# Kernel optimization log

Hardware: AMD Instinct MI355X
Metric: run time of the kernel (lower is better)

## Reference

```python
import jax, jax.numpy as jnp
import numpy as np

D_MODEL = 1024
HEADS = 16
SCALE = float(np.sqrt(D_MODEL / HEADS))  # sqrt(d_k) = sqrt(64) = 8


def setup_inputs() -> dict:
    key = jax.random.key(0)
    ks = jax.random.split(key, 5)
    B, S, D = 4, 2048, D_MODEL
    q = jax.random.normal(ks[0], (B, S, D), dtype=jnp.float32)
    init = 0.02
    wq = jax.random.normal(ks[1], (D, D), dtype=jnp.float32) * init
    wk = jax.random.normal(ks[2], (D, D), dtype=jnp.float32) * init
    wv = jax.random.normal(ks[3], (D, D), dtype=jnp.float32) * init
    wo = jax.random.normal(ks[4], (D, D), dtype=jnp.float32) * init
    return {"q": q, "wq": wq, "wk": wk, "wv": wv, "wo": wo}


def reference(q, wq, wk, wv, wo):
    # Faithful to the source: NO head split is ever performed.
    B, S, D = q.shape
    # nn.Linear convention: y = x @ W.T, weight is [out, in]
    Q = jnp.einsum('bsd,ed->bse', q, wq)
    K = jnp.einsum('bsd,ed->bse', q, wk)
    V = jnp.einsum('bsd,ed->bse', q, wv)
    scores = jnp.einsum('bqe,bke->bqk', Q, K) / SCALE  # [B, S, S]
    attn = jax.nn.softmax(scores, axis=-1)
    out = jnp.einsum('bqk,bke->bqe', attn, V)  # [B, S, D]
    # Source bug reproduced: transpose(1,2).contiguous().view(B, S, -1)
    # => reshape the [B, D, S] contiguous buffer back to [B, S, D].
    out = jnp.transpose(out, (0, 2, 1)).reshape(B, S, D)
    return jnp.einsum('bsd,ed->bse', out, wo)
```

## Files before the change

kernel.cpp:

```cpp
#include <hip/hip_runtime.h>
#include <hip/hip_bf16.h>
#include <stdint.h>

typedef __bf16 bf16;
typedef __attribute__((ext_vector_type(8))) __bf16 bf16x8;
typedef __attribute__((ext_vector_type(4))) float f32x4;
typedef __attribute__((ext_vector_type(8))) unsigned short u16x8;

#define LDS_U32 __attribute__((address_space(3))) uint32_t
#define GLB_U32 const __attribute__((address_space(1))) uint32_t
#define GLOAD16(g, l) __builtin_amdgcn_global_load_lds((GLB_U32*)(g), (LDS_U32*)(l), 16, 0, 0)

#define DSR(dst, addr, OFFLIT) \
  asm volatile("ds_read_b128 %0, %1 offset:" OFFLIT : "=v"(dst) : "v"(addr))

#define WAIT_LGKM0() asm volatile("s_waitcnt lgkmcnt(0)")
#define WAIT_VM(n)   asm volatile("s_waitcnt vmcnt(" #n ")")

__global__ __launch_bounds__(256) void cvt_all(const float* __restrict__ q,
                                               const float* __restrict__ wq,
                                               const float* __restrict__ wk,
                                               const float* __restrict__ wv,
                                               const float* __restrict__ wo,
                                               bf16* __restrict__ qb,
                                               bf16* __restrict__ W3,
                                               bf16* __restrict__ wob) {
  const int b = blockIdx.x;
  const float* src;
  bf16* dst;
  int within;
  if (b < 2048) { src = q; dst = qb; within = b; }
  else {
    const int seg = (b - 2048) >> 8;
    within = (b - 2048) & 255;
    if (seg == 0)      { src = wq; dst = W3; }
    else if (seg == 1) { src = wk; dst = W3 + 1048576; }
    else if (seg == 2) { src = wv; dst = W3 + 2097152; }
    else               { src = wo; dst = wob; }
  }
  const int off = within * 1024;
#pragma unroll
  for (int it = 0; it < 4; ++it) {
    const int j = off + it * 256 + threadIdx.x;
    float4 v = reinterpret_cast<const float4*>(src)[j];
    ushort4 o;
    o.x = __builtin_bit_cast(unsigned short, (bf16)v.x);
    o.y = __builtin_bit_cast(unsigned short, (bf16)v.y);
    o.z = __builtin_bit_cast(unsigned short, (bf16)v.z);
    o.w = __builtin_bit_cast(unsigned short, (bf16)v.w);
    reinterpret_cast<ushort4*>(dst)[j] = o;
  }
}

template <int EPI, int WN>
__global__ __launch_bounds__(512, 2) void g256(const bf16* __restrict__ A,
                                               const bf16* __restrict__ Bm,
                                               void* __restrict__ Cp,
                                               int K, float alpha,
                                               long sA, long sB, long sC, int ldc) {
  constexpr int BN = WN * 64;
  __shared__ bf16 smem_[(32768 + WN * 8192) / 2];
  const long z = blockIdx.z;
  const int t = threadIdx.x;
  const int l = t & 63;
  const int w = t >> 6;
  const int wr = (w >> 2) * 128;
  const int wc = (w & 3) * (WN * 16);
  const int NT = K >> 6;

  const bf16* Ab = A + z * sA + (long)(blockIdx.y * 256) * K;
  const bf16* Bb = Bm + z * sB + (long)(blockIdx.x * BN) * K;

  uint32_t loc = (uint32_t)t * 16u;
  uint32_t g0 = loc ^ (((loc >> 9) & 1u) << 5);
  const int r0 = (int)(((g0 >> 10) >> 1) * 16 + ((g0 >> 6) & 15));
  const int c0 = (int)(((g0 >> 10) & 1) * 32 + ((g0 & 63) >> 1));

  uint32_t lo_ = (uint32_t)((l & 15) * 64 + (l >> 4) * 16);
  const uint32_t lane_off = lo_ ^ (((lo_ >> 9) & 1u) << 5);
  const uint32_t aRegion = (uint32_t)(wr >> 7) * 16384u;
  const uint32_t smem_base = (uint32_t)(size_t)&smem_[0];
  const uint32_t aAddr = smem_base + aRegion + lane_off;

  uint32_t bA[WN];
#pragma unroll
  for (int n = 0; n < WN; ++n) {
    const uint32_t row = (uint32_t)(wc + n * 16);
    bA[n] = smem_base + 32768u + (row >> 6) * 8192u + ((row & 63u) >> 4) * 2048u + lane_off;
  }

  auto STAGE1 = [&](const bf16* mat, int unit, int tile, uint32_t isB) {
    uint32_t dst = isB + (uint32_t)unit * 8192u + (uint32_t)t * 16u;
    const bf16* src = mat + (long)(unit * 64 + r0) * K + tile * 64 + c0;
    GLOAD16(src, smem_ + (dst >> 1));
  };

  f32x4 acc[8][WN] = {};

  STAGE1(Ab, 0, 0, 0u); STAGE1(Ab, 1, 0, 0u); STAGE1(Ab, 2, 0, 0u); STAGE1(Ab, 3, 0, 0u);
#pragma unroll
  for (int u = 0; u < WN; ++u) STAGE1(Bb, u, 0, 32768u);
  __builtin_amdgcn_sched_barrier(0);
  WAIT_VM(0);
  __builtin_amdgcn_s_barrier();

#define MFMAPH(ph)                                                                   \
  _Pragma("unroll") for (int mi = 0; mi < 2; ++mi)                                   \
  _Pragma("unroll") for (int n = 0; n < WN; ++n)                                     \
  _Pragma("unroll") for (int kk = 0; kk < 2; ++kk)                                   \
    acc[(ph) * 2 + mi][n] = __builtin_amdgcn_mfma_f32_16x16x32_bf16(                 \
        __builtin_bit_cast(bf16x8, aF[mi][kk]), __builtin_bit_cast(bf16x8, bF[n][kk]), \
        acc[(ph) * 2 + mi][n], 0, 0, 0);

  for (int T = 0; T < NT; ++T) {
    f32x4 bF[WN][2];
    f32x4 aF[2][2];

#pragma unroll
    for (int n = 0; n < WN; ++n) {
      DSR(bF[n][0], bA[n], "0");
      DSR(bF[n][1], bA[n], "1024");
    }
    DSR(aF[0][0], aAddr, "0");    DSR(aF[0][1], aAddr, "1024");
    DSR(aF[1][0], aAddr, "2048"); DSR(aF[1][1], aAddr, "3072");
    __builtin_amdgcn_sched_barrier(0);
    __builtin_amdgcn_s_barrier();
    WAIT_LGKM0();
    __builtin_amdgcn_sched_barrier(0);
    __builtin_amdgcn_s_setprio(1);
    MFMAPH(0)
    __builtin_amdgcn_s_setprio(0);
    __builtin_amdgcn_s_barrier();

    {
      const uint32_t aP = aAddr + 4096u;
      DSR(aF[0][0], aP, "0");    DSR(aF[0][1], aP, "1024");
      DSR(aF[1][0], aP, "2048"); DSR(aF[1][1], aP, "3072");
      if (T + 1 < NT) {
#pragma unroll
        for (int u = 0; u < WN; ++u) STAGE1(Bb, u, T + 1, 32768u);
      }
      __builtin_amdgcn_sched_barrier(0);
      __builtin_amdgcn_s_barrier();
      WAIT_LGKM0();
      __builtin_amdgcn_sched_barrier(0);
      __builtin_amdgcn_s_setprio(1);
      MFMAPH(1)
      __builtin_amdgcn_s_setprio(0);
      __builtin_amdgcn_sched_barrier(0);
      if (T + 1 < NT) {
        if constexpr (WN == 2) { WAIT_VM(2); }
        else if constexpr (WN == 3) { WAIT_VM(3); }
        else { WAIT_VM(4); }
      } else {
        WAIT_VM(0);
      }
      __builtin_amdgcn_sched_barrier(0);
      __builtin_amdgcn_s_barrier();
    }

    {
      const uint32_t aP = aAddr + 8192u;
      DSR(aF[0][0], aP, "0");    DSR(aF[0][1], aP, "1024");
      DSR(aF[1][0], aP, "2048"); DSR(aF[1][1], aP, "3072");
      if (T + 1 < NT) { STAGE1(Ab, 0, T + 1, 0u); STAGE1(Ab, 2, T + 1, 0u); }
      __builtin_amdgcn_sched_barrier(0);
      __builtin_amdgcn_s_barrier();
      WAIT_LGKM0();
      __builtin_amdgcn_sched_barrier(0);
      __builtin_amdgcn_s_setprio(1);
      MFMAPH(2)
      __builtin_amdgcn_s_setprio(0);
      __builtin_amdgcn_s_barrier();
    }

    {
      const uint32_t aP = aAddr + 12288u;
      DSR(aF[0][0], aP, "0");    DSR(aF[0][1], aP, "1024");
      DSR(aF[1][0], aP, "2048"); DSR(aF[1][1], aP, "3072");
      __builtin_amdgcn_sched_barrier(0);
      __builtin_amdgcn_s_barrier();
      WAIT_LGKM0();
      __builtin_amdgcn_sched_barrier(0);
      __builtin_amdgcn_s_setprio(1);
      MFMAPH(3)
      __builtin_amdgcn_s_setprio(0);
      __builtin_amdgcn_s_barrier();
    }

    if (T + 1 < NT) { STAGE1(Ab, 1, T + 1, 0u); STAGE1(Ab, 3, T + 1, 0u); }
    __builtin_amdgcn_sched_barrier(0);
    if (T + 1 < NT) { WAIT_VM(2); } else { WAIT_VM(0); }
    __builtin_amdgcn_sched_barrier(0);
    __builtin_amdgcn_s_barrier();
  }
#undef MFMAPH

  const int orow0 = blockIdx.y * 256 + wr + (l >> 4) * 4;
  const int ocol0 = blockIdx.x * BN + wc + (l & 15);
#pragma unroll
  for (int m = 0; m < 8; ++m)
#pragma unroll
    for (int n = 0; n < WN; ++n)
#pragma unroll
      for (int i = 0; i < 4; ++i) {
        const long r = orow0 + m * 16 + i;
        const long c = ocol0 + n * 16;
        const float v = acc[m][n][i] * alpha;
        if constexpr (EPI == 0) {
          ((bf16*)Cp)[z * sC + r * ldc + c] = (bf16)v;
        } else if constexpr (EPI == 2) {
          ((float*)Cp)[r * ldc + c] = v;
        } else if constexpr (EPI == 4) {
          ((bf16*)Cp)[(r >> 11) * 2097152 + c * 2048 + (r & 2047)] = (bf16)v;
        } else {
          bf16* Qb = (bf16*)Cp;
          bf16* Kb = Qb + 8388608;
          if (c < 1024) Qb[r * 1024 + c] = (bf16)v;
          else Kb[r * 1024 + (c - 1024)] = (bf16)v;
        }
      }
}

__global__ __launch_bounds__(256) void softmax_rows(bf16* __restrict__ P) {
  const long row = blockIdx.x;
  bf16* p = P + row * 2048;
  const int t = threadIdx.x;
  const int lane = t & 63;
  const int wave = t >> 6;

  u16x8 raw = *reinterpret_cast<const u16x8*>(p + t * 8);
  float v[8];
#pragma unroll
  for (int j = 0; j < 8; ++j) {
    uint32_t bits = ((uint32_t)raw[j]) << 16;
    v[j] = __builtin_bit_cast(float, bits);
  }
  float m = v[0];
#pragma unroll
  for (int j = 1; j < 8; ++j) m = fmaxf(m, v[j]);
#pragma unroll
  for (int off = 32; off > 0; off >>= 1) m = fmaxf(m, __shfl_xor(m, off, 64));
  __shared__ float redm[4];
  __shared__ float reds[4];
  if (lane == 0) redm[wave] = m;
  __syncthreads();
  m = fmaxf(fmaxf(redm[0], redm[1]), fmaxf(redm[2], redm[3]));

  float s = 0.f;
#pragma unroll
  for (int j = 0; j < 8; ++j) {
    v[j] = __expf(v[j] - m);
    s += v[j];
  }
#pragma unroll
  for (int off = 32; off > 0; off >>= 1) s += __shfl_xor(s, off, 64);
  if (lane == 0) reds[wave] = s;
  __syncthreads();
  s = reds[0] + reds[1] + reds[2] + reds[3];
  const float inv = 1.f / s;

  u16x8 o;
#pragma unroll
  for (int j = 0; j < 8; ++j) o[j] = __builtin_bit_cast(unsigned short, (bf16)(v[j] * inv));
  *reinterpret_cast<u16x8*>(p + t * 8) = o;
}

extern "C" void kernel_launch(void* const* d_in, const int* in_sizes, int n_in,
                              void* d_out, int out_size, void* d_ws, size_t ws_size,
                              hipStream_t stream) {
  const float* q = (const float*)d_in[0];
  const float* wq = (const float*)d_in[1];
  const float* wk = (const float*)d_in[2];
  const float* wv = (const float*)d_in[3];
  const float* wo = (const float*)d_in[4];
  float* out = (float*)d_out;

  constexpr int B = 4, S = 2048, D = 1024;
  constexpr long SD = (long)S * D;
  constexpr long SS = (long)S * S;
  constexpr long DD = (long)D * D;

  bf16* wsb = (bf16*)d_ws;
  bf16* qb = wsb;
  bf16* W3 = qb + B * SD;
  bf16* wob = W3 + 3 * DD;
  bf16* Qb = wob + DD;
  bf16* Kb = Qb + B * SD;
  bf16* Vt = Kb + B * SD;
  bf16* P = Vt + B * SD;
  bf16* X = P + B * SS;

  cvt_all<<<3072, 256, 0, stream>>>(q, wq, wk, wv, wo, qb, W3, wob);

  g256<5, 4><<<dim3(8, 32, 1), 512, 0, stream>>>(qb, W3, Qb, D, 1.f, 0, 0, 0, 0);
  g256<4, 2><<<dim3(8, 32, 1), 512, 0, stream>>>(qb, W3 + 2 * DD, Vt, D, 1.f, 0, 0, 0, 0);
  g256<0, 4><<<dim3(8, 8, B), 512, 0, stream>>>(Qb, Kb, P, D, 0.125f, SD, SD, SS, S);
  softmax_rows<<<B * S, 256, 0, stream>>>(P);
  g256<0, 2><<<dim3(16, 4, B), 512, 0, stream>>>(Vt, P, X, S, 1.f, SD, SS, SD, S);
  g256<2, 2><<<dim3(8, 32, 1), 512, 0, stream>>>(X, wob, out, D, 1.f, 0, 0, 0, D);
}
```

Before: 207.4 us.

## Double-buffer GEMM LDS tiles and collapse per-phase barriers into one per K-step

The main GEMM kernel's single shared-memory tile is replaced by two ping-pong buffers indexed by K-tile parity. Global-to-LDS loads for tile T+1 are issued at the start of step T. The four MFMA phases become two larger phases of eight A fragment reads each. Only one vmcnt(0) wait and one barrier remain per K iteration, which removes most of the intra-iteration s_barrier synchronisation. The cost is double the LDS footprint, which may prevent two 512-thread blocks from fitting per CU as the launch bounds assume, and the finer-grained waves interleaving of the old schedule is lost.

```diff
diff --git a/kernel.cpp b/kernel.cpp
--- a/kernel.cpp
+++ b/kernel.cpp
@@ -15,7 +15,7 @@
   asm volatile("ds_read_b128 %0, %1 offset:" OFFLIT : "=v"(dst) : "v"(addr))
 
 #define WAIT_LGKM0() asm volatile("s_waitcnt lgkmcnt(0)")
-#define WAIT_VM(n)   asm volatile("s_waitcnt vmcnt(" #n ")")
+#define WAIT_VM0()   asm volatile("s_waitcnt vmcnt(0)")
 
 __global__ __launch_bounds__(256) void cvt_all(const float* __restrict__ q,
                                                const float* __restrict__ wq,
@@ -59,7 +59,8 @@
                                                int K, float alpha,
                                                long sA, long sB, long sC, int ldc) {
   constexpr int BN = WN * 64;
-  __shared__ bf16 smem_[(32768 + WN * 8192) / 2];
+  constexpr uint32_t PARB = 32768u + WN * 8192u;
+  __shared__ bf16 smem_[PARB];
   const long z = blockIdx.z;
   const int t = threadIdx.x;
   const int l = t & 63;
@@ -80,7 +81,7 @@
   const uint32_t lane_off = lo_ ^ (((lo_ >> 9) & 1u) << 5);
   const uint32_t aRegion = (uint32_t)(wr >> 7) * 16384u;
   const uint32_t smem_base = (uint32_t)(size_t)&smem_[0];
-  const uint32_t aAddr = smem_base + aRegion + lane_off;
+  const uint32_t aBase = smem_base + aRegion + lane_off;
 
   uint32_t bA[WN];
 #pragma unroll
@@ -90,7 +91,7 @@
   }
 
   auto STAGE1 = [&](const bf16* mat, int unit, int tile, uint32_t isB) {
-    uint32_t dst = isB + (uint32_t)unit * 8192u + (uint32_t)t * 16u;
+    uint32_t dst = (uint32_t)(tile & 1) * PARB + isB + (uint32_t)unit * 8192u + (uint32_t)t * 16u;
     const bf16* src = mat + (long)(unit * 64 + r0) * K + tile * 64 + c0;
     GLOAD16(src, smem_ + (dst >> 1));
   };
@@ -101,100 +102,73 @@
 #pragma unroll
   for (int u = 0; u < WN; ++u) STAGE1(Bb, u, 0, 32768u);
   __builtin_amdgcn_sched_barrier(0);
-  WAIT_VM(0);
+  WAIT_VM0();
   __builtin_amdgcn_s_barrier();
 
-#define MFMAPH(ph)                                                                   \
-  _Pragma("unroll") for (int mi = 0; mi < 2; ++mi)                                   \
-  _Pragma("unroll") for (int n = 0; n < WN; ++n)                                     \
-  _Pragma("unroll") for (int kk = 0; kk < 2; ++kk)                                   \
-    acc[(ph) * 2 + mi][n] = __builtin_amdgcn_mfma_f32_16x16x32_bf16(                 \
-        __builtin_bit_cast(bf16x8, aF[mi][kk]), __builtin_bit_cast(bf16x8, bF[n][kk]), \
-        acc[(ph) * 2 + mi][n], 0, 0, 0);
-
   for (int T = 0; T < NT; ++T) {
+    const uint32_t pb = (uint32_t)(T & 1) * PARB;
+    const uint32_t aA = aBase + pb;
     f32x4 bF[WN][2];
-    f32x4 aF[2][2];
+    f32x4 aF[2][2][2];
 
 #pragma unroll
     for (int n = 0; n < WN; ++n) {
-      DSR(bF[n][0], bA[n], "0");
-      DSR(bF[n][1], bA[n], "1024");
+      DSR(bF[n][0], bA[n] + pb, "0");
+      DSR(bF[n][1], bA[n] + pb, "1024");
     }
-    DSR(aF[0][0], aAddr, "0");    DSR(aF[0][1], aAddr, "1024");
-    DSR(aF[1][0], aAddr, "2048"); DSR(aF[1][1], aAddr, "3072");
-    __builtin_amdgcn_sched_barrier(0);
+    DSR(aF[0][0][0], aA, "0");    DSR(aF[0][0][1], aA, "1024");
+    DSR(aF[0][1][0], aA, "2048"); DSR(aF[0][1][1], aA, "3072");
+    DSR(aF[1][0][0], aA, "4096"); DSR(aF[1][0][1], aA, "5120");
+    DSR(aF[1][1][0], aA, "6144"); DSR(aF[1][1][1], aA, "7168");
+    if (T + 1 < NT) {
+#pragma unroll
+      for (int u = 0; u < WN; ++u) STAGE1(Bb, u, T + 1, 32768u);
+      STAGE1(Ab, 0, T + 1, 0u); STAGE1(Ab, 1, T + 1, 0u);
+    }
+    __builtin_amdgcn_sched_barrier(0);
+    WAIT_LGKM0();
+    __builtin_amdgcn_sched_barrier(0);
+    __builtin_amdgcn_s_setprio(1);
+#pragma unroll
+    for (int q = 0; q < 2; ++q)
+#pragma unroll
+      for (int mi = 0; mi < 2; ++mi)
+#pragma unroll
+        for (int n = 0; n < WN; ++n)
+#pragma unroll
+          for (int kk = 0; kk < 2; ++kk)
+            acc[q * 2 + mi][n] = __builtin_amdgcn_mfma_f32_16x16x32_bf16(
+                __builtin_bit_cast(bf16x8, aF[q][mi][kk]), __builtin_bit_cast(bf16x8, bF[n][kk]),
+                acc[q * 2 + mi][n], 0, 0, 0);
+    __builtin_amdgcn_s_setprio(0);
+    __builtin_amdgcn_sched_barrier(0);
+
+    DSR(aF[0][0][0], aA, "8192");  DSR(aF[0][0][1], aA, "9216");
+    DSR(aF[0][1][0], aA, "10240"); DSR(aF[0][1][1], aA, "11264");
+    DSR(aF[1][0][0], aA, "12288"); DSR(aF[1][0][1], aA, "13312");
+    DSR(aF[1][1][0], aA, "14336"); DSR(aF[1][1][1], aA, "15360");
+    if (T + 1 < NT) { STAGE1(Ab, 2, T + 1, 0u); STAGE1(Ab, 3, T + 1, 0u); }
+    __builtin_amdgcn_sched_barrier(0);
+    WAIT_LGKM0();
+    __builtin_amdgcn_sched_barrier(0);
+    __builtin_amdgcn_s_setprio(1);
+#pragma unroll
+    for (int q = 0; q < 2; ++q)
+#pragma unroll
+      for (int mi = 0; mi < 2; ++mi)
+#pragma unroll
+        for (int n = 0; n < WN; ++n)
+#pragma unroll
+          for (int kk = 0; kk < 2; ++kk)
+            acc[4 + q * 2 + mi][n] = __builtin_amdgcn_mfma_f32_16x16x32_bf16(
+                __builtin_bit_cast(bf16x8, aF[q][mi][kk]), __builtin_bit_cast(bf16x8, bF[n][kk]),
+                acc[4 + q * 2 + mi][n], 0, 0, 0);
+    __builtin_amdgcn_s_setprio(0);
+    __builtin_amdgcn_sched_barrier(0);
+
+    WAIT_VM0();
     __builtin_amdgcn_s_barrier();
-    WAIT_LGKM0();
-    __builtin_amdgcn_sched_barrier(0);
-    __builtin_amdgcn_s_setprio(1);
-    MFMAPH(0)
-    __builtin_amdgcn_s_setprio(0);
-    __builtin_amdgcn_s_barrier();
-
-    {
-      const uint32_t aP = aAddr + 4096u;
-      DSR(aF[0][0], aP, "0");    DSR(aF[0][1], aP, "1024");
-      DSR(aF[1][0], aP, "2048"); DSR(aF[1][1], aP, "3072");
-      if (T + 1 < NT) {
-#pragma unroll
-        for (int u = 0; u < WN; ++u) STAGE1(Bb, u, T + 1, 32768u);
-      }
-      __builtin_amdgcn_sched_barrier(0);
-      __builtin_amdgcn_s_barrier();
-      WAIT_LGKM0();
-      __builtin_amdgcn_sched_barrier(0);
-      __builtin_amdgcn_s_setprio(1);
-      MFMAPH(1)
-      __builtin_amdgcn_s_setprio(0);
-      __builtin_amdgcn_sched_barrier(0);
-      if (T + 1 < NT) {
-        if constexpr (WN == 2) { WAIT_VM(2); }
-        else if constexpr (WN == 3) { WAIT_VM(3); }
-        else { WAIT_VM(4); }
-      } else {
-        WAIT_VM(0);
-      }
-      __builtin_amdgcn_sched_barrier(0);
-      __builtin_amdgcn_s_barrier();
-    }
-
-    {
-      const uint32_t aP = aAddr + 8192u;
-      DSR(aF[0][0], aP, "0");    DSR(aF[0][1], aP, "1024");
-      DSR(aF[1][0], aP, "2048"); DSR(aF[1][1], aP, "3072");
-      if (T + 1 < NT) { STAGE1(Ab, 0, T + 1, 0u); STAGE1(Ab, 2, T + 1, 0u); }
-      __builtin_amdgcn_sched_barrier(0);
-      __builtin_amdgcn_s_barrier();
-      WAIT_LGKM0();
-      __builtin_amdgcn_sched_barrier(0);
-      __builtin_amdgcn_s_setprio(1);
-      MFMAPH(2)
-      __builtin_amdgcn_s_setprio(0);
-      __builtin_amdgcn_s_barrier();
-    }
-
-    {
-      const uint32_t aP = aAddr + 12288u;
-      DSR(aF[0][0], aP, "0");    DSR(aF[0][1], aP, "1024");
-      DSR(aF[1][0], aP, "2048"); DSR(aF[1][1], aP, "3072");
-      __builtin_amdgcn_sched_barrier(0);
-      __builtin_amdgcn_s_barrier();
-      WAIT_LGKM0();
-      __builtin_amdgcn_sched_barrier(0);
-      __builtin_amdgcn_s_setprio(1);
-      MFMAPH(3)
-      __builtin_amdgcn_s_setprio(0);
-      __builtin_amdgcn_s_barrier();
-    }
-
-    if (T + 1 < NT) { STAGE1(Ab, 1, T + 1, 0u); STAGE1(Ab, 3, T + 1, 0u); }
-    __builtin_amdgcn_sched_barrier(0);
-    if (T + 1 < NT) { WAIT_VM(2); } else { WAIT_VM(0); }
-    __builtin_amdgcn_sched_barrier(0);
-    __builtin_amdgcn_s_barrier();
-  }
-#undef MFMAPH
+  }
 
   const int orow0 = blockIdx.y * 256 + wr + (l >> 4) * 4;
   const int ocol0 = blockIdx.x * BN + wc + (l & 15);
```

New measurement: 203.7 us. No clear change (-1.8%).
